# Optimization experiments

Hardware: AMD Instinct MI355X
Metric: run time of the kernel (lower is better)

The kernel has to match this reference:

```python
import jax, jax.numpy as jnp
import numpy as np

J = 16384
D = 2048

def setup_inputs() -> dict:
    key = jax.random.key(0)
    embeddings = jax.random.normal(key, (J, D), dtype=jnp.float32)
    return {"embeddings": embeddings}

def reference(embeddings) -> jnp.ndarray:
    J_, d = embeddings.shape
    # position indices j=1..J, feature indices k=1..d (as in the torch loop)
    j = jnp.arange(1, J_ + 1, dtype=embeddings.dtype)  # [J]
    k = jnp.arange(1, d + 1, dtype=embeddings.dtype)   # [d]
    a = 1.0 - j / J_            # [J]
    b = 1.0 - 2.0 * j / J_      # [J]
    # L[j,k] = (1 - j/J) - (k/d)*(1 - 2j/J)
    L = a[:, None] - (k / d)[None, :] * b[:, None]  # [J, d]
    return jnp.sum(L * embeddings, axis=0)  # [d]
```

## Files before the change

kernel.cpp:

```cpp
#include <hip/hip_runtime.h>


constexpr int D_COLS = 2048;
constexpr int J_ROWS = 16384;
constexpr int T1  = 512;
constexpr int NB1 = 1024;
constexpr int RPB = J_ROWS / NB1;
constexpr int NB2 = 64;

__global__ __launch_bounds__(T1, 8) void pe_stage1(const float* __restrict__ E,
                                                   float* __restrict__ ws) {
    const int tid  = threadIdx.x;
    const int col0 = tid * 4;
    const int b    = blockIdx.x;
    const int row0 = b * RPB;
    const float invJ = 1.0f / (float)J_ROWS;
    const float invD = 1.0f / (float)D_COLS;
    const float c0 = (float)(col0 + 1) * invD;
    const float c1 = (float)(col0 + 2) * invD;
    const float c2 = (float)(col0 + 3) * invD;
    const float c3 = (float)(col0 + 4) * invD;

    const float* base = E + (size_t)row0 * D_COLS + col0;

    float4 acc = make_float4(0.f, 0.f, 0.f, 0.f);
    #pragma unroll 1
    for (int it = 0; it < RPB / 4; ++it) {
        const int r = it * 4;
        const float4 e0 = *reinterpret_cast<const float4*>(base + (size_t)(r + 0) * D_COLS);
        const float4 e1 = *reinterpret_cast<const float4*>(base + (size_t)(r + 1) * D_COLS);
        const float4 e2 = *reinterpret_cast<const float4*>(base + (size_t)(r + 2) * D_COLS);
        const float4 e3 = *reinterpret_cast<const float4*>(base + (size_t)(r + 3) * D_COLS);

        const float j0 = (float)(row0 + r + 1);
        const float j1 = j0 + 1.0f, j2 = j0 + 2.0f, j3 = j0 + 3.0f;
        const float a0 = fmaf(-j0, invJ, 1.0f), bb0 = fmaf(-2.f * j0, invJ, 1.0f);
        const float a1 = fmaf(-j1, invJ, 1.0f), bb1 = fmaf(-2.f * j1, invJ, 1.0f);
        const float a2 = fmaf(-j2, invJ, 1.0f), bb2 = fmaf(-2.f * j2, invJ, 1.0f);
        const float a3 = fmaf(-j3, invJ, 1.0f), bb3 = fmaf(-2.f * j3, invJ, 1.0f);

        acc.x = fmaf(fmaf(-c0, bb0, a0), e0.x, acc.x);
        acc.y = fmaf(fmaf(-c1, bb0, a0), e0.y, acc.y);
        acc.z = fmaf(fmaf(-c2, bb0, a0), e0.z, acc.z);
        acc.w = fmaf(fmaf(-c3, bb0, a0), e0.w, acc.w);
        acc.x = fmaf(fmaf(-c0, bb1, a1), e1.x, acc.x);
        acc.y = fmaf(fmaf(-c1, bb1, a1), e1.y, acc.y);
        acc.z = fmaf(fmaf(-c2, bb1, a1), e1.z, acc.z);
        acc.w = fmaf(fmaf(-c3, bb1, a1), e1.w, acc.w);
        acc.x = fmaf(fmaf(-c0, bb2, a2), e2.x, acc.x);
        acc.y = fmaf(fmaf(-c1, bb2, a2), e2.y, acc.y);
        acc.z = fmaf(fmaf(-c2, bb2, a2), e2.z, acc.z);
        acc.w = fmaf(fmaf(-c3, bb2, a2), e2.w, acc.w);
        acc.x = fmaf(fmaf(-c0, bb3, a3), e3.x, acc.x);
        acc.y = fmaf(fmaf(-c1, bb3, a3), e3.y, acc.y);
        acc.z = fmaf(fmaf(-c2, bb3, a3), e3.z, acc.z);
        acc.w = fmaf(fmaf(-c3, bb3, a3), e3.w, acc.w);
    }

    *reinterpret_cast<float4*>(ws + (size_t)b * D_COLS + col0) = acc;
}

__global__ __launch_bounds__(T1) void pe_stage2(const float* __restrict__ ws,
                                                float* __restrict__ ws2) {
    const int col0 = threadIdx.x * 4;
    const int b    = blockIdx.x;
    const float* base = ws + (size_t)(b * (NB1 / NB2)) * D_COLS + col0;
    float4 acc = make_float4(0.f, 0.f, 0.f, 0.f);
    #pragma unroll
    for (int r = 0; r < NB1 / NB2; ++r) {
        const float4 v = *reinterpret_cast<const float4*>(base + (size_t)r * D_COLS);
        acc.x += v.x; acc.y += v.y; acc.z += v.z; acc.w += v.w;
    }
    *reinterpret_cast<float4*>(ws2 + (size_t)b * D_COLS + col0) = acc;
}

__global__ __launch_bounds__(T1) void pe_stage3(const float* __restrict__ ws2,
                                                float* __restrict__ out) {
    const int k = blockIdx.x * T1 + threadIdx.x;
    float s0 = 0.f, s1 = 0.f, s2 = 0.f, s3 = 0.f;
    #pragma unroll
    for (int r = 0; r < NB2; r += 4) {
        s0 += ws2[(size_t)(r + 0) * D_COLS + k];
        s1 += ws2[(size_t)(r + 1) * D_COLS + k];
        s2 += ws2[(size_t)(r + 2) * D_COLS + k];
        s3 += ws2[(size_t)(r + 3) * D_COLS + k];
    }
    out[k] = (s0 + s1) + (s2 + s3);
}

extern "C" void kernel_launch(void* const* d_in, const int* in_sizes, int n_in,
                              void* d_out, int out_size, void* d_ws, size_t ws_size,
                              hipStream_t stream) {
    const float* E = (const float*)d_in[0];
    float* out = (float*)d_out;
    float* ws  = (float*)d_ws;
    float* ws2 = ws + (size_t)NB1 * D_COLS;
    (void)in_sizes; (void)n_in; (void)out_size; (void)ws_size;

    pe_stage1<<<NB1, T1, 0, stream>>>(E, ws);
    pe_stage2<<<NB2, T1, 0, stream>>>(ws, ws2);
    pe_stage3<<<D_COLS / T1, T1, 0, stream>>>(ws2, out);
}
```

Measured before the change: 194.2 us.

## Stream rows via async global-to-LDS loads with per-wave double buffering

Stage 1 is restructured so each wave owns whole rows, which are strided across all waves. The rows are fetched with global_load_lds directly into per-wave double-buffered shared memory, with explicit vmcnt waits so the next row's loads overlap the current row's FMAs. The four waves' partial sums are then combined in LDS before one write per block. The goal is deeper memory-level parallelism on a bandwidth-bound reduction, at the cost of 64KB LDS per block, which limits occupancy, and hand-written wait counts that depend on the compiler's instruction ordering.

```diff
diff --git a/kernel.cpp b/kernel.cpp
--- a/kernel.cpp
+++ b/kernel.cpp
@@ -3,80 +3,116 @@
 
 constexpr int D_COLS = 2048;
 constexpr int J_ROWS = 16384;
-constexpr int T1  = 512;
+constexpr int TB1 = 256;
 constexpr int NB1 = 1024;
-constexpr int RPB = J_ROWS / NB1;
+constexpr int NWAVES = NB1 * (TB1 / 64);
 constexpr int NB2 = 64;
+constexpr int T2T3 = 512;
 
-__global__ __launch_bounds__(T1, 8) void pe_stage1(const float* __restrict__ E,
-                                                   float* __restrict__ ws) {
-    const int tid  = threadIdx.x;
-    const int col0 = tid * 4;
-    const int b    = blockIdx.x;
-    const int row0 = b * RPB;
+typedef float vf4 __attribute__((ext_vector_type(4)));
+
+#define GLOBAL_AS __attribute__((address_space(1)))
+#define LDS_AS    __attribute__((address_space(3)))
+#define WAIT_VMCNT(N) asm volatile("s_waitcnt vmcnt(%0)" ::"n"(N) : "memory")
+
+__global__ __launch_bounds__(TB1) void pe_stage1(const float* __restrict__ E,
+                                                 float* __restrict__ ws) {
+    __shared__ float smem[4 * 2 * D_COLS];
+    const int lane = threadIdx.x & 63;
+    const int wv   = threadIdx.x >> 6;
+    const int gw   = blockIdx.x * 4 + wv;
+    const int bufA = wv * 2 * D_COLS;
+    const int bufB = bufA + D_COLS;
+
     const float invJ = 1.0f / (float)J_ROWS;
     const float invD = 1.0f / (float)D_COLS;
-    const float c0 = (float)(col0 + 1) * invD;
-    const float c1 = (float)(col0 + 2) * invD;
-    const float c2 = (float)(col0 + 3) * invD;
-    const float c3 = (float)(col0 + 4) * invD;
 
-    const float* base = E + (size_t)row0 * D_COLS + col0;
-
-    float4 acc = make_float4(0.f, 0.f, 0.f, 0.f);
-    #pragma unroll 1
-    for (int it = 0; it < RPB / 4; ++it) {
-        const int r = it * 4;
-        const float4 e0 = *reinterpret_cast<const float4*>(base + (size_t)(r + 0) * D_COLS);
-        const float4 e1 = *reinterpret_cast<const float4*>(base + (size_t)(r + 1) * D_COLS);
-        const float4 e2 = *reinterpret_cast<const float4*>(base + (size_t)(r + 2) * D_COLS);
-        const float4 e3 = *reinterpret_cast<const float4*>(base + (size_t)(r + 3) * D_COLS);
-
-        const float j0 = (float)(row0 + r + 1);
-        const float j1 = j0 + 1.0f, j2 = j0 + 2.0f, j3 = j0 + 3.0f;
-        const float a0 = fmaf(-j0, invJ, 1.0f), bb0 = fmaf(-2.f * j0, invJ, 1.0f);
-        const float a1 = fmaf(-j1, invJ, 1.0f), bb1 = fmaf(-2.f * j1, invJ, 1.0f);
-        const float a2 = fmaf(-j2, invJ, 1.0f), bb2 = fmaf(-2.f * j2, invJ, 1.0f);
-        const float a3 = fmaf(-j3, invJ, 1.0f), bb3 = fmaf(-2.f * j3, invJ, 1.0f);
-
-        acc.x = fmaf(fmaf(-c0, bb0, a0), e0.x, acc.x);
-        acc.y = fmaf(fmaf(-c1, bb0, a0), e0.y, acc.y);
-        acc.z = fmaf(fmaf(-c2, bb0, a0), e0.z, acc.z);
-        acc.w = fmaf(fmaf(-c3, bb0, a0), e0.w, acc.w);
-        acc.x = fmaf(fmaf(-c0, bb1, a1), e1.x, acc.x);
-        acc.y = fmaf(fmaf(-c1, bb1, a1), e1.y, acc.y);
-        acc.z = fmaf(fmaf(-c2, bb1, a1), e1.z, acc.z);
-        acc.w = fmaf(fmaf(-c3, bb1, a1), e1.w, acc.w);
-        acc.x = fmaf(fmaf(-c0, bb2, a2), e2.x, acc.x);
-        acc.y = fmaf(fmaf(-c1, bb2, a2), e2.y, acc.y);
-        acc.z = fmaf(fmaf(-c2, bb2, a2), e2.z, acc.z);
-        acc.w = fmaf(fmaf(-c3, bb2, a2), e2.w, acc.w);
-        acc.x = fmaf(fmaf(-c0, bb3, a3), e3.x, acc.x);
-        acc.y = fmaf(fmaf(-c1, bb3, a3), e3.y, acc.y);
-        acc.z = fmaf(fmaf(-c2, bb3, a3), e3.z, acc.z);
-        acc.w = fmaf(fmaf(-c3, bb3, a3), e3.w, acc.w);
+    vf4 c[8], acc[8];
+    #pragma unroll
+    for (int i = 0; i < 8; ++i) {
+        const int col = i * 256 + lane * 4;
+        c[i].x = (float)(col + 1) * invD;
+        c[i].y = (float)(col + 2) * invD;
+        c[i].z = (float)(col + 3) * invD;
+        c[i].w = (float)(col + 4) * invD;
+        acc[i] = (vf4)0.f;
     }
 
-    *reinterpret_cast<float4*>(ws + (size_t)b * D_COLS + col0) = acc;
+    auto issue_row = [&](int buf, int row) {
+        const float* g = E + (size_t)row * D_COLS + lane * 4;
+        #pragma unroll
+        for (int i = 0; i < 8; ++i) {
+            __builtin_amdgcn_global_load_lds(
+                (const GLOBAL_AS void*)(g + i * 256),
+                (LDS_AS void*)&smem[buf + i * 256],
+                16, 0, 0);
+        }
+    };
+
+    auto consume = [&](int buf, int row) {
+        const float jf = (float)(row + 1);
+        const float aa = fmaf(-jf, invJ, 1.0f);
+        const float bb = fmaf(-2.0f * jf, invJ, 1.0f);
+        #pragma unroll
+        for (int i = 0; i < 8; ++i) {
+            const vf4 e = *(const vf4*)&smem[buf + i * 256 + lane * 4];
+            vf4 w;
+            w.x = fmaf(-c[i].x, bb, aa);
+            w.y = fmaf(-c[i].y, bb, aa);
+            w.z = fmaf(-c[i].z, bb, aa);
+            w.w = fmaf(-c[i].w, bb, aa);
+            acc[i].x = fmaf(w.x, e.x, acc[i].x);
+            acc[i].y = fmaf(w.y, e.y, acc[i].y);
+            acc[i].z = fmaf(w.z, e.z, acc[i].z);
+            acc[i].w = fmaf(w.w, e.w, acc[i].w);
+        }
+    };
+
+    issue_row(bufA, gw);
+    issue_row(bufB, NWAVES + gw);
+    WAIT_VMCNT(8);
+    consume(bufA, gw);
+    issue_row(bufA, 2 * NWAVES + gw);
+    WAIT_VMCNT(8);
+    consume(bufB, NWAVES + gw);
+    issue_row(bufB, 3 * NWAVES + gw);
+    WAIT_VMCNT(8);
+    consume(bufA, 2 * NWAVES + gw);
+    WAIT_VMCNT(0);
+    consume(bufB, 3 * NWAVES + gw);
+
+    #pragma unroll
+    for (int i = 0; i < 8; ++i)
+        *(vf4*)&smem[wv * 2 * D_COLS + i * 256 + lane * 4] = acc[i];
+    __syncthreads();
+
+    const int t = threadIdx.x;
+    #pragma unroll
+    for (int m = 0; m < 2; ++m) {
+        const int col = m * 1024 + t * 4;
+        vf4 s = *(const vf4*)&smem[0 * 2 * D_COLS + col];
+        s += *(const vf4*)&smem[1 * 2 * D_COLS + col];
+        s += *(const vf4*)&smem[2 * 2 * D_COLS + col];
+        s += *(const vf4*)&smem[3 * 2 * D_COLS + col];
+        *(vf4*)&ws[(size_t)blockIdx.x * D_COLS + col] = s;
+    }
 }
 
-__global__ __launch_bounds__(T1) void pe_stage2(const float* __restrict__ ws,
-                                                float* __restrict__ ws2) {
+__global__ __launch_bounds__(T2T3) void pe_stage2(const float* __restrict__ ws,
+                                                  float* __restrict__ ws2) {
     const int col0 = threadIdx.x * 4;
     const int b    = blockIdx.x;
     const float* base = ws + (size_t)(b * (NB1 / NB2)) * D_COLS + col0;
-    float4 acc = make_float4(0.f, 0.f, 0.f, 0.f);
+    vf4 acc = (vf4)0.f;
     #pragma unroll
-    for (int r = 0; r < NB1 / NB2; ++r) {
-        const float4 v = *reinterpret_cast<const float4*>(base + (size_t)r * D_COLS);
-        acc.x += v.x; acc.y += v.y; acc.z += v.z; acc.w += v.w;
-    }
-    *reinterpret_cast<float4*>(ws2 + (size_t)b * D_COLS + col0) = acc;
+    for (int r = 0; r < NB1 / NB2; ++r)
+        acc += *(const vf4*)(base + (size_t)r * D_COLS);
+    *(vf4*)(ws2 + (size_t)b * D_COLS + col0) = acc;
 }
 
-__global__ __launch_bounds__(T1) void pe_stage3(const float* __restrict__ ws2,
-                                                float* __restrict__ out) {
-    const int k = blockIdx.x * T1 + threadIdx.x;
+__global__ __launch_bounds__(T2T3) void pe_stage3(const float* __restrict__ ws2,
+                                                  float* __restrict__ out) {
+    const int k = blockIdx.x * T2T3 + threadIdx.x;
     float s0 = 0.f, s1 = 0.f, s2 = 0.f, s3 = 0.f;
     #pragma unroll
     for (int r = 0; r < NB2; r += 4) {
@@ -97,7 +133,7 @@
     float* ws2 = ws + (size_t)NB1 * D_COLS;
     (void)in_sizes; (void)n_in; (void)out_size; (void)ws_size;
 
-    pe_stage1<<<NB1, T1, 0, stream>>>(E, ws);
-    pe_stage2<<<NB2, T1, 0, stream>>>(ws, ws2);
-    pe_stage3<<<D_COLS / T1, T1, 0, stream>>>(ws2, out);
+    pe_stage1<<<NB1, TB1, 0, stream>>>(E, ws);
+    pe_stage2<<<NB2, T2T3, 0, stream>>>(ws, ws2);
+    pe_stage3<<<D_COLS / T2T3, T2T3, 0, stream>>>(ws2, out);
 }
```

Result: no change. 191.3 us (-1.5%).
